# Kernel tuning notes

Hardware: AMD Instinct MI355X
Metric: run time of the kernel (lower is better)

Reference implementation:

```python
import jax, jax.numpy as jnp
import numpy as np

H = 1024
V = 50257
S = 8192


def setup_inputs() -> dict:
    key = jax.random.key(0)
    ks = jax.random.split(key, 13)
    s = 0.02  # param init scale
    return {
        "input": jax.random.randint(ks[0], (1,), 0, V),
        "hidden": jax.random.normal(ks[1], (1, 1, H), jnp.float32),
        "encoder_outputs": jax.random.normal(ks[2], (S, H), jnp.float32),
        "embedding": jax.random.normal(ks[3], (V, H), jnp.float32) * s,
        "attn_w": jax.random.normal(ks[4], (1, 2 * H), jnp.float32) * s,
        "attn_b": jnp.zeros((1,), jnp.float32),
        "comb_w": jax.random.normal(ks[5], (H, 2 * H), jnp.float32) * s,
        "comb_b": jnp.zeros((H,), jnp.float32),
        "w_ih": jax.random.normal(ks[6], (3 * H, H), jnp.float32) * s,
        "w_hh": jax.random.normal(ks[7], (3 * H, H), jnp.float32) * s,
        "b_ih": jnp.zeros((3 * H,), jnp.float32),
        "b_hh": jnp.zeros((3 * H,), jnp.float32),
        "out_w": jax.random.normal(ks[8], (V, H), jnp.float32) * s,
        "out_b": jnp.zeros((V,), jnp.float32),
    }


def reference(input, hidden, encoder_outputs, embedding, attn_w, attn_b,
              comb_w, comb_b, w_ih, w_hh, b_ih, b_hh, out_w, out_b):
    # embedded = embedding(input).view(1,1,-1); dropout in eval mode = identity
    emb = embedding[input[0]]            # [H]
    h0 = hidden[0, 0]                    # [H]
    # Original loop computes the SAME score attn(cat(emb, hidden)) for every
    # timestep -> softmax over a constant vector (uniform weights). Compute the
    # scalar once and broadcast (same math, one GEMV instead of S launches).
    score = jnp.concatenate([emb, h0]) @ attn_w[0] + attn_b[0]   # scalar
    seq_len = encoder_outputs.shape[0]
    attn_weights = jax.nn.softmax(jnp.broadcast_to(score, (seq_len,)))  # [S]
    attn_applied = attn_weights @ encoder_outputs                # [H]
    combined = jnp.concatenate([emb, attn_applied]) @ comb_w.T + comb_b  # [H]
    x = jax.nn.relu(combined)
    # Single GRU step (torch nn.GRU gate math)
    gi = w_ih @ x + b_ih                 # [3H]
    gh = w_hh @ h0 + b_hh                # [3H]
    i_r, i_z, i_n = jnp.split(gi, 3)
    h_r, h_z, h_n = jnp.split(gh, 3)
    r = jax.nn.sigmoid(i_r + h_r)
    z = jax.nn.sigmoid(i_z + h_z)
    n = jnp.tanh(i_n + r * h_n)
    h_new = (1.0 - z) * n + z * h0       # [H]
    logits = h_new @ out_w.T + out_b     # [V]
    output = jax.nn.log_softmax(logits)[None, :]   # [1, V]
    return output, h_new[None, None, :], attn_weights[None, :]
```

## Files before the change

kernel.cpp:

```cpp
#include <hip/hip_runtime.h>
#include <math.h>

#define HN 1024
#define VN 50257
#define SN 8192

#define WS_PARTIAL 0
#define WS_AA      262144
#define WS_X       263168
#define WS_G       264192
#define WS_HNEW    270336
#define WS_LOGITS  271360
#define WS_EXPD    321618

__device__ __forceinline__ float wred(float v) {
#pragma unroll
  for (int m = 32; m; m >>= 1) v += __shfl_xor(v, m);
  return v;
}

__device__ __forceinline__ float dot4(float4 a, float4 b) {
  return a.x * b.x + a.y * b.y + a.z * b.z + a.w * b.w;
}

__global__ __launch_bounds__(1024) void k1_front(
    const float* __restrict__ enc, const float* __restrict__ w_hh,
    const float* __restrict__ hidden, float* __restrict__ ws,
    float* __restrict__ out_attn) {
  const int blk = blockIdx.x, t = threadIdx.x;
  if (blk < 256) {
    __shared__ float4 lds[1024];
    const int g = t >> 8, c4 = t & 255;
    const float4* e4 = (const float4*)enc + ((size_t)blk * 32 + g * 8) * 256 + c4;
    float4 acc = make_float4(0.f, 0.f, 0.f, 0.f);
#pragma unroll
    for (int r = 0; r < 8; ++r) {
      float4 v = e4[r * 256];
      acc.x += v.x; acc.y += v.y; acc.z += v.z; acc.w += v.w;
    }
    lds[t] = acc;
    __syncthreads();
    if (t < 256) {
      float4 a = lds[t], b = lds[t + 256], c = lds[t + 512], d = lds[t + 768];
      float4 s = make_float4(a.x + b.x + c.x + d.x, a.y + b.y + c.y + d.y,
                             a.z + b.z + c.z + d.z, a.w + b.w + c.w + d.w);
      ((float4*)(ws + WS_PARTIAL))[blk * 256 + t] = s;
    }
    if (t < 32) out_attn[blk * 32 + t] = 1.f / 8192.f;
  } else {
    const int wg = (blk - 256) * 16 + (t >> 6);
    const int l = t & 63;
    const float4* h4 = (const float4*)hidden;
    float4 hv0 = h4[l], hv1 = h4[64 + l], hv2 = h4[128 + l], hv3 = h4[192 + l];
#pragma unroll
    for (int k = 0; k < 3; ++k) {
      const int r = wg + k * 1024;
      const float4* m4 = (const float4*)w_hh + (size_t)r * 256;
      float acc = dot4(m4[l], hv0) + dot4(m4[64 + l], hv1) +
                  dot4(m4[128 + l], hv2) + dot4(m4[192 + l], hv3);
      acc = wred(acc);
      if (l == 0) ws[WS_G + 3072 + r] = acc;
    }
  }
}

__global__ void k2_reduce(float* __restrict__ ws) {
  __shared__ float lds[256];
  const int t = threadIdx.x, b = blockIdx.x;
  const int c = b * 32 + (t & 31), rg = t >> 5;
  const float* p = ws + WS_PARTIAL;
  float s = 0.f;
#pragma unroll 8
  for (int j = 0; j < 32; ++j) s += p[(rg * 32 + j) * 1024 + c];
  lds[t] = s;
  __syncthreads();
  if (t < 32) {
    float a = 0.f;
#pragma unroll
    for (int j = 0; j < 8; ++j) a += lds[j * 32 + t];
    ws[WS_AA + b * 32 + t] = a * (1.f / 8192.f);
  }
}

__global__ void k3_combined(const int* __restrict__ token,
                            const float* __restrict__ embedding,
                            const float* __restrict__ comb_w,
                            const float* __restrict__ comb_b,
                            float* __restrict__ ws) {
  const int w = threadIdx.x >> 6, l = threadIdx.x & 63;
  const int i = blockIdx.x * 4 + w;
  const int tok = token[0];
  const float4* emb4 = (const float4*)embedding + (size_t)tok * 256;
  const float4* aa4 = (const float4*)(ws + WS_AA);
  const float4* cw4 = (const float4*)comb_w + (size_t)i * 512;
  float acc = 0.f;
#pragma unroll
  for (int k = 0; k < 8; ++k) {
    float4 wv = cw4[k * 64 + l];
    float4 xv = (k < 4) ? emb4[k * 64 + l] : aa4[(k - 4) * 64 + l];
    acc += dot4(wv, xv);
  }
  acc = wred(acc);
  if (l == 0) {
    float c = acc + comb_b[i];
    ws[WS_X + i] = fmaxf(c, 0.f);
  }
}

__global__ void k4_gates(const float* __restrict__ w_ih, float* __restrict__ ws) {
  const int w = threadIdx.x >> 6, l = threadIdx.x & 63;
  const int r = blockIdx.x * 4 + w;
  const float4* m4 = (const float4*)w_ih + (size_t)r * 256;
  const float4* x4 = (const float4*)(ws + WS_X);
  float acc = 0.f;
#pragma unroll
  for (int k = 0; k < 4; ++k) acc += dot4(m4[k * 64 + l], x4[k * 64 + l]);
  acc = wred(acc);
  if (l == 0) ws[WS_G + r] = acc;
}

__global__ void k4b_hnew(const float* __restrict__ b_ih, const float* __restrict__ b_hh,
                         const float* __restrict__ hidden, float* __restrict__ ws,
                         float* __restrict__ d_out) {
  const int t = threadIdx.x;
  const float* g = ws + WS_G;
#pragma unroll
  for (int j = 0; j < 4; ++j) {
    const int i = t + j * 256;
    float ir = g[i] + b_ih[i];
    float iz = g[i + 1024] + b_ih[i + 1024];
    float inn = g[i + 2048] + b_ih[i + 2048];
    float hr = g[3072 + i] + b_hh[i];
    float hz = g[3072 + i + 1024] + b_hh[i + 1024];
    float hn = g[3072 + i + 2048] + b_hh[i + 2048];
    float rg = 1.f / (1.f + expf(-(ir + hr)));
    float zg = 1.f / (1.f + expf(-(iz + hz)));
    float ng = tanhf(inn + rg * hn);
    float h = (1.f - zg) * ng + zg * hidden[i];
    ws[WS_HNEW + i] = h;
    d_out[VN + i] = h;
  }
}

__global__ void k5_logits(const float* __restrict__ out_w, const float* __restrict__ out_b,
                          float* __restrict__ ws) {
  const int blk = blockIdx.x, t = threadIdx.x;
  const int w = t >> 6, l = t & 63;
  const int gw = blk * 4 + w;
  const float4* h4p = (const float4*)(ws + WS_HNEW);
  float4 h0_ = h4p[l], h1_ = h4p[64 + l], h2_ = h4p[128 + l], h3_ = h4p[192 + l];
  const float4* ow4 = (const float4*)out_w;
  double eacc = 0.0;
  for (int v = gw; v < VN; v += 16384) {
    const int v2 = v + 8192;
    const bool ok2 = (v2 < VN);
    const float4* r0 = ow4 + (size_t)v * 256;
    const float4* r1 = ow4 + (size_t)(ok2 ? v2 : v) * 256;
    float acc0 = dot4(r0[l], h0_) + dot4(r0[64 + l], h1_) +
                 dot4(r0[128 + l], h2_) + dot4(r0[192 + l], h3_);
    float acc1 = dot4(r1[l], h0_) + dot4(r1[64 + l], h1_) +
                 dot4(r1[128 + l], h2_) + dot4(r1[192 + l], h3_);
    acc0 = wred(acc0);
    acc1 = wred(acc1);
    if (l == 0) {
      float lg0 = acc0 + out_b[v];
      ws[WS_LOGITS + v] = lg0;
      eacc += (double)expf(lg0);
      if (ok2) {
        float lg1 = acc1 + out_b[v2];
        ws[WS_LOGITS + v2] = lg1;
        eacc += (double)expf(lg1);
      }
    }
  }
  __shared__ double sd[4];
  if (l == 0) sd[w] = eacc;
  __syncthreads();
  if (t == 0) ((double*)(ws + WS_EXPD))[blk] = sd[0] + sd[1] + sd[2] + sd[3];
}

__global__ void k6_final(const float* __restrict__ ws, float* __restrict__ d_out) {
  __shared__ double sd[256];
  const int t = threadIdx.x;
  const double* ed = (const double*)(ws + WS_EXPD);
  double a = 0.0;
#pragma unroll
  for (int j = 0; j < 8; ++j) a += ed[t + j * 256];
  sd[t] = a;
  __syncthreads();
  for (int s = 128; s; s >>= 1) {
    if (t < s) sd[t] += sd[t + s];
    __syncthreads();
  }
  const float logZ = (float)log(sd[0]);
  const int v = blockIdx.x * 256 + t;
  if (v < VN) d_out[v] = ws[WS_LOGITS + v] - logZ;
}

extern "C" void kernel_launch(void* const* d_in, const int* in_sizes, int n_in,
                              void* d_out, int out_size, void* d_ws, size_t ws_size,
                              hipStream_t stream) {
  const int* token = (const int*)d_in[0];
  const float* hidden = (const float*)d_in[1];
  const float* enc = (const float*)d_in[2];
  const float* embedding = (const float*)d_in[3];
  const float* comb_w = (const float*)d_in[6];
  const float* comb_b = (const float*)d_in[7];
  const float* w_ih = (const float*)d_in[8];
  const float* w_hh = (const float*)d_in[9];
  const float* b_ih = (const float*)d_in[10];
  const float* b_hh = (const float*)d_in[11];
  const float* out_w = (const float*)d_in[12];
  const float* out_b = (const float*)d_in[13];
  float* out = (float*)d_out;
  float* ws = (float*)d_ws;

  k1_front<<<320, 1024, 0, stream>>>(enc, w_hh, hidden, ws, out + VN + HN);
  k2_reduce<<<32, 256, 0, stream>>>(ws);
  k3_combined<<<256, 256, 0, stream>>>(token, embedding, comb_w, comb_b, ws);
  k4_gates<<<768, 256, 0, stream>>>(w_ih, ws);
  k4b_hnew<<<1, 256, 0, stream>>>(b_ih, b_hh, hidden, ws, out);
  k5_logits<<<2048, 256, 0, stream>>>(out_w, out_b, ws);
  k6_final<<<197, 256, 0, stream>>>(ws, out);
}
```

Measured before the change: 63.76 us.

## Hoist embedding half of combine into front kernel and fuse GRU gates with update

The embedding half of the combine GEMV moves into the first kernel as extra blocks, so only the attention half stays on the critical path after the reduction. The w_ih gate GEMV is fused with the GRU update: each wave computes the r, z and n rows for one index and applies the gate math directly. This removes the single-block k4b kernel and one launch. The logits kernel is restructured into a fixed unrolled loop of three rows per wave plus a tail, with h staged through LDS, to raise memory-level parallelism.

```diff
diff --git a/kernel.cpp b/kernel.cpp
--- a/kernel.cpp
+++ b/kernel.cpp
@@ -8,7 +8,8 @@
 #define WS_PARTIAL 0
 #define WS_AA      262144
 #define WS_X       263168
-#define WS_G       264192
+#define WS_GH      264192
+#define WS_CEMB    267264
 #define WS_HNEW    270336
 #define WS_LOGITS  271360
 #define WS_EXPD    321618
@@ -25,7 +26,9 @@
 
 __global__ __launch_bounds__(1024) void k1_front(
     const float* __restrict__ enc, const float* __restrict__ w_hh,
-    const float* __restrict__ hidden, float* __restrict__ ws,
+    const float* __restrict__ hidden, const int* __restrict__ token,
+    const float* __restrict__ embedding, const float* __restrict__ comb_w,
+    const float* __restrict__ comb_b, float* __restrict__ ws,
     float* __restrict__ out_attn) {
   const int blk = blockIdx.x, t = threadIdx.x;
   if (blk < 256) {
@@ -47,7 +50,7 @@
       ((float4*)(ws + WS_PARTIAL))[blk * 256 + t] = s;
     }
     if (t < 32) out_attn[blk * 32 + t] = 1.f / 8192.f;
-  } else {
+  } else if (blk < 320) {
     const int wg = (blk - 256) * 16 + (t >> 6);
     const int l = t & 63;
     const float4* h4 = (const float4*)hidden;
@@ -59,8 +62,19 @@
       float acc = dot4(m4[l], hv0) + dot4(m4[64 + l], hv1) +
                   dot4(m4[128 + l], hv2) + dot4(m4[192 + l], hv3);
       acc = wred(acc);
-      if (l == 0) ws[WS_G + 3072 + r] = acc;
-    }
+      if (l == 0) ws[WS_GH + r] = acc;
+    }
+  } else {
+    const int i = (blk - 320) * 16 + (t >> 6);
+    const int l = t & 63;
+    const int tok = token[0];
+    const float4* emb4 = (const float4*)embedding + (size_t)tok * 256;
+    const float4* cw4 = (const float4*)comb_w + (size_t)i * 512;
+    float acc = 0.f;
+#pragma unroll
+    for (int k = 0; k < 4; ++k) acc += dot4(cw4[k * 64 + l], emb4[k * 64 + l]);
+    acc = wred(acc);
+    if (l == 0) ws[WS_CEMB + i] = acc + comb_b[i];
   }
 }
 
@@ -82,57 +96,43 @@
   }
 }
 
-__global__ void k3_combined(const int* __restrict__ token,
-                            const float* __restrict__ embedding,
-                            const float* __restrict__ comb_w,
-                            const float* __restrict__ comb_b,
-                            float* __restrict__ ws) {
+__global__ void k3_x(const float* __restrict__ comb_w, float* __restrict__ ws) {
   const int w = threadIdx.x >> 6, l = threadIdx.x & 63;
   const int i = blockIdx.x * 4 + w;
-  const int tok = token[0];
-  const float4* emb4 = (const float4*)embedding + (size_t)tok * 256;
   const float4* aa4 = (const float4*)(ws + WS_AA);
-  const float4* cw4 = (const float4*)comb_w + (size_t)i * 512;
+  const float4* cw4 = (const float4*)comb_w + (size_t)i * 512 + 256;
   float acc = 0.f;
 #pragma unroll
-  for (int k = 0; k < 8; ++k) {
-    float4 wv = cw4[k * 64 + l];
-    float4 xv = (k < 4) ? emb4[k * 64 + l] : aa4[(k - 4) * 64 + l];
-    acc += dot4(wv, xv);
-  }
+  for (int k = 0; k < 4; ++k) acc += dot4(cw4[k * 64 + l], aa4[k * 64 + l]);
   acc = wred(acc);
+  if (l == 0) ws[WS_X + i] = fmaxf(ws[WS_CEMB + i] + acc, 0.f);
+}
+
+__global__ void k4_gates_h(const float* __restrict__ w_ih,
+                           const float* __restrict__ b_ih, const float* __restrict__ b_hh,
+                           const float* __restrict__ hidden, float* __restrict__ ws,
+                           float* __restrict__ d_out) {
+  const int w = threadIdx.x >> 6, l = threadIdx.x & 63;
+  const int i = blockIdx.x * 4 + w;
+  const float4* x4 = (const float4*)(ws + WS_X);
+  float4 xv0 = x4[l], xv1 = x4[64 + l], xv2 = x4[128 + l], xv3 = x4[192 + l];
+  const float4* m0 = (const float4*)w_ih + (size_t)i * 256;
+  const float4* m1 = (const float4*)w_ih + (size_t)(i + 1024) * 256;
+  const float4* m2 = (const float4*)w_ih + (size_t)(i + 2048) * 256;
+  float a0 = dot4(m0[l], xv0) + dot4(m0[64 + l], xv1) +
+             dot4(m0[128 + l], xv2) + dot4(m0[192 + l], xv3);
+  float a1 = dot4(m1[l], xv0) + dot4(m1[64 + l], xv1) +
+             dot4(m1[128 + l], xv2) + dot4(m1[192 + l], xv3);
+  float a2 = dot4(m2[l], xv0) + dot4(m2[64 + l], xv1) +
+             dot4(m2[128 + l], xv2) + dot4(m2[192 + l], xv3);
+  a0 = wred(a0); a1 = wred(a1); a2 = wred(a2);
   if (l == 0) {
-    float c = acc + comb_b[i];
-    ws[WS_X + i] = fmaxf(c, 0.f);
-  }
-}
-
-__global__ void k4_gates(const float* __restrict__ w_ih, float* __restrict__ ws) {
-  const int w = threadIdx.x >> 6, l = threadIdx.x & 63;
-  const int r = blockIdx.x * 4 + w;
-  const float4* m4 = (const float4*)w_ih + (size_t)r * 256;
-  const float4* x4 = (const float4*)(ws + WS_X);
-  float acc = 0.f;
-#pragma unroll
-  for (int k = 0; k < 4; ++k) acc += dot4(m4[k * 64 + l], x4[k * 64 + l]);
-  acc = wred(acc);
-  if (l == 0) ws[WS_G + r] = acc;
-}
-
-__global__ void k4b_hnew(const float* __restrict__ b_ih, const float* __restrict__ b_hh,
-                         const float* __restrict__ hidden, float* __restrict__ ws,
-                         float* __restrict__ d_out) {
-  const int t = threadIdx.x;
-  const float* g = ws + WS_G;
-#pragma unroll
-  for (int j = 0; j < 4; ++j) {
-    const int i = t + j * 256;
-    float ir = g[i] + b_ih[i];
-    float iz = g[i + 1024] + b_ih[i + 1024];
-    float inn = g[i + 2048] + b_ih[i + 2048];
-    float hr = g[3072 + i] + b_hh[i];
-    float hz = g[3072 + i + 1024] + b_hh[i + 1024];
-    float hn = g[3072 + i + 2048] + b_hh[i + 2048];
+    float ir = a0 + b_ih[i];
+    float iz = a1 + b_ih[i + 1024];
+    float inn = a2 + b_ih[i + 2048];
+    float hr = ws[WS_GH + i] + b_hh[i];
+    float hz = ws[WS_GH + i + 1024] + b_hh[i + 1024];
+    float hn = ws[WS_GH + i + 2048] + b_hh[i + 2048];
     float rg = 1.f / (1.f + expf(-(ir + hr)));
     float zg = 1.f / (1.f + expf(-(iz + hz)));
     float ng = tanhf(inn + rg * hn);
@@ -147,33 +147,48 @@
   const int blk = blockIdx.x, t = threadIdx.x;
   const int w = t >> 6, l = t & 63;
   const int gw = blk * 4 + w;
-  const float4* h4p = (const float4*)(ws + WS_HNEW);
-  float4 h0_ = h4p[l], h1_ = h4p[64 + l], h2_ = h4p[128 + l], h3_ = h4p[192 + l];
+  __shared__ float4 hs4[256];
+  __shared__ double sd[4];
+  if (t < 256) hs4[t] = ((const float4*)(ws + WS_HNEW))[t];
+  __syncthreads();
+  float4 h0_ = hs4[l], h1_ = hs4[64 + l], h2_ = hs4[128 + l], h3_ = hs4[192 + l];
   const float4* ow4 = (const float4*)out_w;
   double eacc = 0.0;
-  for (int v = gw; v < VN; v += 16384) {
-    const int v2 = v + 8192;
-    const bool ok2 = (v2 < VN);
+#pragma unroll
+  for (int it = 0; it < 2; ++it) {
+    const int v0 = gw + it * 24576;
+    const float4* r0 = ow4 + (size_t)v0 * 256;
+    const float4* r1 = r0 + 8192 * 256;
+    const float4* r2 = r1 + 8192 * 256;
+    float a0 = dot4(r0[l], h0_) + dot4(r0[64 + l], h1_) +
+               dot4(r0[128 + l], h2_) + dot4(r0[192 + l], h3_);
+    float a1 = dot4(r1[l], h0_) + dot4(r1[64 + l], h1_) +
+               dot4(r1[128 + l], h2_) + dot4(r1[192 + l], h3_);
+    float a2 = dot4(r2[l], h0_) + dot4(r2[64 + l], h1_) +
+               dot4(r2[128 + l], h2_) + dot4(r2[192 + l], h3_);
+    a0 = wred(a0); a1 = wred(a1); a2 = wred(a2);
+    if (l == 0) {
+      float lg0 = a0 + out_b[v0];
+      float lg1 = a1 + out_b[v0 + 8192];
+      float lg2 = a2 + out_b[v0 + 16384];
+      ws[WS_LOGITS + v0] = lg0;
+      ws[WS_LOGITS + v0 + 8192] = lg1;
+      ws[WS_LOGITS + v0 + 16384] = lg2;
+      eacc += (double)expf(lg0) + (double)expf(lg1) + (double)expf(lg2);
+    }
+  }
+  if (gw < 1105) {
+    const int v = gw + 49152;
     const float4* r0 = ow4 + (size_t)v * 256;
-    const float4* r1 = ow4 + (size_t)(ok2 ? v2 : v) * 256;
-    float acc0 = dot4(r0[l], h0_) + dot4(r0[64 + l], h1_) +
-                 dot4(r0[128 + l], h2_) + dot4(r0[192 + l], h3_);
-    float acc1 = dot4(r1[l], h0_) + dot4(r1[64 + l], h1_) +
-                 dot4(r1[128 + l], h2_) + dot4(r1[192 + l], h3_);
-    acc0 = wred(acc0);
-    acc1 = wred(acc1);
+    float a = dot4(r0[l], h0_) + dot4(r0[64 + l], h1_) +
+              dot4(r0[128 + l], h2_) + dot4(r0[192 + l], h3_);
+    a = wred(a);
     if (l == 0) {
-      float lg0 = acc0 + out_b[v];
-      ws[WS_LOGITS + v] = lg0;
-      eacc += (double)expf(lg0);
-      if (ok2) {
-        float lg1 = acc1 + out_b[v2];
-        ws[WS_LOGITS + v2] = lg1;
-        eacc += (double)expf(lg1);
-      }
-    }
-  }
-  __shared__ double sd[4];
+      float lg = a + out_b[v];
+      ws[WS_LOGITS + v] = lg;
+      eacc += (double)expf(lg);
+    }
+  }
   if (l == 0) sd[w] = eacc;
   __syncthreads();
   if (t == 0) ((double*)(ws + WS_EXPD))[blk] = sd[0] + sd[1] + sd[2] + sd[3];
@@ -215,11 +230,11 @@
   float* out = (float*)d_out;
   float* ws = (float*)d_ws;
 
-  k1_front<<<320, 1024, 0, stream>>>(enc, w_hh, hidden, ws, out + VN + HN);
+  k1_front<<<384, 1024, 0, stream>>>(enc, w_hh, hidden, token, embedding,
+                                     comb_w, comb_b, ws, out + VN + HN);
   k2_reduce<<<32, 256, 0, stream>>>(ws);
-  k3_combined<<<256, 256, 0, stream>>>(token, embedding, comb_w, comb_b, ws);
-  k4_gates<<<768, 256, 0, stream>>>(w_ih, ws);
-  k4b_hnew<<<1, 256, 0, stream>>>(b_ih, b_hh, hidden, ws, out);
+  k3_x<<<256, 256, 0, stream>>>(comb_w, ws);
+  k4_gates_h<<<256, 256, 0, stream>>>(w_ih, b_ih, b_hh, hidden, ws, out);
   k5_logits<<<2048, 256, 0, stream>>>(out_w, out_b, ws);
   k6_final<<<197, 256, 0, stream>>>(ws, out);
 }
```

New measurement: 60.87 us. 1.05x faster.
